# Kernel tuning notes

Measured on AMD Instinct MI355X. Metric: run time of the kernel, lower is better.

## Reference

```python
import jax, jax.numpy as jnp
import numpy as np

E = 8        # n_experts
K = 2        # top_k
D = 1024     # n_embed
H = 2048     # moe_n_hidden
B, T = 4, 2048


def setup_inputs() -> dict:
    key = jax.random.key(0)
    ks = jax.random.split(key, 6)
    s = 0.02
    return {
        "x": jax.random.normal(ks[0], (B, T, D), dtype=jnp.float32),
        "Wr": jax.random.normal(ks[1], (D, E), dtype=jnp.float32) * s,   # router weight
        "W1": jax.random.normal(ks[2], (E, D, 2 * H), dtype=jnp.float32) * s,
        "b1": jnp.zeros((E, 2 * H), dtype=jnp.float32),
        "W2": jax.random.normal(ks[3], (E, H, D), dtype=jnp.float32) * s,
        "b2": jnp.zeros((E, D), dtype=jnp.float32),
    }


def reference(x, Wr, W1, b1, W2, b2):
    b, t, d = x.shape
    # router logits (noise=0, temp=1.0)
    z = jnp.einsum('btd,de->bte', x, Wr)                 # [B,T,E]
    vals, idx = jax.lax.top_k(z, K)                      # [B,T,K]
    gates = jax.nn.softmax(vals, axis=-1)                # [B,T,K]
    # combine weights per (token, expert): sum_k gate_k * 1[idx_k == e]
    onehot = jax.nn.one_hot(idx, E, dtype=x.dtype)       # [B,T,K,E]
    comb = jnp.einsum('btk,btke->bte', gates, onehot).reshape(b * t, E)
    xf = x.reshape(b * t, d)                             # [N,D]
    out = jnp.zeros_like(xf)
    for e in range(E):  # fixed small loop over structurally-distinct experts
        ab = xf @ W1[e] + b1[e]                          # [N,2H]
        a, bb = jnp.split(ab, 2, axis=-1)
        h = jax.nn.silu(a) * bb                          # swiGLU
        y = h @ W2[e] + b2[e]                            # [N,D]
        out = out + comb[:, e:e + 1] * y
    return out.reshape(b, t, d)
```

## Files before the change

### kernel.cpp

```cpp
#include <hip/hip_runtime.h>


#define N_TOK 8192
#define DIM   1024
#define HID   2048
#define NEXP  8
#define NK    (N_TOK * 2)
#define MAXT2 72
#define MAXT1 136

typedef __attribute__((ext_vector_type(8))) short short8;
typedef __attribute__((ext_vector_type(4))) float f32x4;

#define BARX() __builtin_amdgcn_s_barrier()
#define FEN()  asm volatile("" ::: "memory")
#define VMW4() asm volatile("s_waitcnt vmcnt(4)" ::: "memory")
#define VMW2() asm volatile("s_waitcnt vmcnt(2)" ::: "memory")
#define VMW0() asm volatile("s_waitcnt vmcnt(0)" ::: "memory")
#define PRIO(p) __builtin_amdgcn_s_setprio(p)

static __device__ __forceinline__ unsigned short f2bf(float f) {
  unsigned int u = __float_as_uint(f);
  u += 0x7fffu + ((u >> 16) & 1u);
  return (unsigned short)(u >> 16);
}

static __device__ __forceinline__ void glds16(const void* g, void* l) {
  __builtin_amdgcn_global_load_lds(
      (const __attribute__((address_space(1))) unsigned int*)g,
      (__attribute__((address_space(3))) unsigned int*)l, 16, 0, 0);
}

__device__ __forceinline__ void transpose_tile(const float* __restrict__ s,
                                               unsigned short* __restrict__ d,
                                               int R, int C, int c0, int r0,
                                               unsigned short (*tT)[68]) {
  int tid = threadIdx.x;
  int c = tid & 63, rq = tid >> 6;
#pragma unroll
  for (int q = 0; q < 4; ++q) {
    int rb = q * 16 + rq * 4;
    ushort4 v;
    v.x = f2bf(s[(size_t)(r0 + rb + 0) * C + c0 + c]);
    v.y = f2bf(s[(size_t)(r0 + rb + 1) * C + c0 + c]);
    v.z = f2bf(s[(size_t)(r0 + rb + 2) * C + c0 + c]);
    v.w = f2bf(s[(size_t)(r0 + rb + 3) * C + c0 + c]);
    *(ushort4*)&tT[c][rb] = v;
  }
  __syncthreads();
#pragma unroll
  for (int it = 0; it < 4; ++it) {
    int idx = it * 256 + tid;
    int cc = idx >> 4;
    int r4 = (idx & 15) * 4;
    *(ushort4*)(d + (size_t)(c0 + cc) * R + r0 + r4) = *(const ushort4*)&tT[cc][r4];
  }
}

__global__ __launch_bounds__(256) void prep_k(
    const float* __restrict__ x, const float* __restrict__ Wr,
    const float* __restrict__ W1, const float* __restrict__ W2,
    unsigned short* __restrict__ w1t, unsigned short* __restrict__ w2t,
    unsigned short* __restrict__ xb, int* __restrict__ te,
    float* __restrict__ tg, float* __restrict__ out) {
  __shared__ unsigned short tT[64][68];
  int bid = blockIdx.x;
  if (bid < 8192) {
    int z = bid >> 10, rem = bid & 1023;
    int c0 = (rem & 63) * 64, r0 = (rem >> 6) * 64;
    transpose_tile(W1 + (size_t)z * DIM * 2 * HID,
                   w1t + (size_t)z * DIM * 2 * HID, DIM, 2 * HID, c0, r0, tT);
  } else if (bid < 12288) {
    int b2 = bid - 8192;
    int z = b2 >> 9, rem = b2 & 511;
    int c0 = (rem & 15) * 64, r0 = (rem >> 4) * 64;
    transpose_tile(W2 + (size_t)z * HID * DIM,
                   w2t + (size_t)z * HID * DIM, HID, DIM, c0, r0, tT);
  } else if (bid < 14336) {
    int n = (bid - 12288) * 4 + (threadIdx.x >> 6);
    int lane = threadIdx.x & 63;
    float z[8];
#pragma unroll
    for (int e = 0; e < 8; ++e) z[e] = 0.f;
    const float* xr = x + (size_t)n * DIM;
    unsigned short* xbr = xb + (size_t)n * DIM;
#pragma unroll 4
    for (int i = 0; i < DIM / 64; ++i) {
      int d = lane + i * 64;
      float xv = xr[d];
      xbr[d] = f2bf(xv);
      float4 w0 = *(const float4*)(Wr + (size_t)d * 8);
      float4 w1 = *(const float4*)(Wr + (size_t)d * 8 + 4);
      z[0] += xv * w0.x; z[1] += xv * w0.y; z[2] += xv * w0.z; z[3] += xv * w0.w;
      z[4] += xv * w1.x; z[5] += xv * w1.y; z[6] += xv * w1.z; z[7] += xv * w1.w;
    }
    for (int off = 32; off; off >>= 1)
#pragma unroll
      for (int e = 0; e < 8; ++e) z[e] += __shfl_down(z[e], off);
    if (lane == 0) {
      int e0 = 0; float v0 = z[0];
#pragma unroll
      for (int e = 1; e < 8; ++e) if (z[e] > v0) { v0 = z[e]; e0 = e; }
      int e1 = -1; float v1 = -3.4e38f;
#pragma unroll
      for (int e = 0; e < 8; ++e) if (e != e0 && z[e] > v1) { v1 = z[e]; e1 = e; }
      float r = expf(v1 - v0);
      float s0 = 1.f / (1.f + r);
      te[n * 2] = e0; te[n * 2 + 1] = e1;
      tg[n * 2] = s0; tg[n * 2 + 1] = r * s0;
    }
  } else {
    int t = bid - 14336;
    float4* o4 = (float4*)out;
    int idx = t * 256 + threadIdx.x;
#pragma unroll
    for (int i = 0; i < 4; ++i) o4[idx + i * 524288] = (float4){0.f, 0.f, 0.f, 0.f};
  }
}

__global__ __launch_bounds__(1024) void sortscan_k(
    const int* __restrict__ te, const float* __restrict__ tg,
    int* __restrict__ offs, int* __restrict__ tl256, int* __restrict__ tl128,
    int* __restrict__ rows, float* __restrict__ rowg) {
  __shared__ int hist[8];
  __shared__ int curs[8];
  int tid = threadIdx.x;
  if (tid < 8) hist[tid] = 0;
  __syncthreads();
  for (int i = tid; i < NK; i += 1024) atomicAdd(&hist[te[i]], 1);
  __syncthreads();
  if (tid == 0) {
    int o = 0, t2 = 0, t1 = 0;
    offs[0] = 0; tl256[0] = 0; tl128[0] = 0;
    for (int e = 0; e < NEXP; ++e) {
      curs[e] = o;
      o += hist[e];
      offs[e + 1] = o;
      t2 += (hist[e] + 255) >> 8;
      tl256[e + 1] = t2;
      t1 += (hist[e] + 127) >> 7;
      tl128[e + 1] = t1;
    }
  }
  __syncthreads();
  for (int i = tid; i < NK; i += 1024) {
    int e = te[i];
    int pos = atomicAdd(&curs[e], 1);
    rows[pos] = i >> 1;
    rowg[pos] = tg[i];
  }
}

template <int GID, int BM>
__global__ __launch_bounds__(512, 2) void moe_gemm8p(
    const unsigned short* __restrict__ Asrc,
    const unsigned short* __restrict__ Wt,
    const float* __restrict__ bias,
    unsigned short* __restrict__ hb,
    float* __restrict__ out,
    const int* __restrict__ rows,
    const float* __restrict__ rowg,
    const int* __restrict__ offs,
    const int* __restrict__ tl) {
  constexpr int KD = (GID == 0) ? DIM : HID;
  constexpr int NT = KD / 64;
  constexpr int MF = BM / 32;
  constexpr int HBIT = BM / 4;
  constexpr int AG = BM / 128;
  constexpr int ASZ = BM * 64;
  __shared__ unsigned short smem[2 * ASZ + 2 * 16384];

  int bt = blockIdx.x;
  if (bt >= tl[NEXP]) return;
  int e = 0;
  while (e < NEXP - 1 && bt >= tl[e + 1]) ++e;
  int rt = bt - tl[e];
  int base = offs[e];
  int cntE = offs[e + 1] - base;
  int row0 = rt * BM;
  int jb = blockIdx.y;

  int tid = threadIdx.x, lane = tid & 63, w = tid >> 6;
  int wr = w >> 2, wc = w & 3;

  int g8 = (((lane & 7) ^ ((lane >> 3) & 7)) * 8);
  const unsigned short* aP[2][AG];
  const unsigned short* bP[2][2];
  int aD[2][AG], bD[2][2];
#pragma unroll
  for (int hf = 0; hf < 2; ++hf) {
#pragma unroll
    for (int s = 0; s < AG; ++s) {
      int q0 = w * (BM / 16) + s * 8;
      int rbA = (q0 < HBIT ? q0 : q0 + HBIT) + hf * HBIT;
      int rA = rbA + (lane >> 3);
      int rr = row0 + rA; rr = rr < cntE ? rr : cntE - 1;
      if (GID == 0) {
        int tok = rows[base + rr];
        aP[hf][s] = Asrc + (size_t)tok * DIM + g8;
      } else {
        aP[hf][s] = Asrc + (size_t)(base + rr) * HID + g8;
      }
      aD[hf][s] = rbA * 64;
    }
#pragma unroll
    for (int s = 0; s < 2; ++s) {
      int q0 = w * 16 + s * 8;
      int rB = hf * 128 + q0 + (lane >> 3);
      if (GID == 0) {
        int j0h = jb * 128;
        int hcol = j0h + (rB >> 5) * 16 + (rB & 15);
        int w1row = hcol + ((rB >> 4) & 1) * HID;
        bP[hf][s] = Wt + ((size_t)e * 2 * HID + w1row) * DIM + g8;
      } else {
        int j0 = jb * 256;
        bP[hf][s] = Wt + ((size_t)e * DIM + (j0 + rB)) * HID + g8;
      }
      bD[hf][s] = (hf * 128 + q0) * 64;
    }
  }

  auto stA = [&](int t, int hf) {
    if (t < NT) {
#pragma unroll
      for (int s = 0; s < AG; ++s)
        glds16(aP[hf][s] + (size_t)t * 64, smem + (t & 1) * ASZ + aD[hf][s]);
    }
  };
  auto stB = [&](int t, int hf) {
    if (t < NT) {
#pragma unroll
      for (int s = 0; s < 2; ++s)
        glds16(bP[hf][s] + (size_t)t * 64, smem + 2 * ASZ + (t & 1) * 16384 + bD[hf][s]);
    }
  };

  int arow = wr * (BM / 2) + (lane & 15);
  int brow = wc * 64 + (lane & 15);
  int kg = lane >> 4, sx = lane & 7;
  unsigned aoffs[2] = {(unsigned)(arow * 64 + ((kg ^ sx) * 8)),
                       (unsigned)(arow * 64 + (((4 + kg) ^ sx) * 8))};
  unsigned boffs[2] = {(unsigned)(brow * 64 + ((kg ^ sx) * 8)),
                       (unsigned)(brow * 64 + (((4 + kg) ^ sx) * 8))};

  f32x4 acc[MF][4];
#pragma unroll
  for (int m = 0; m < MF; ++m)
#pragma unroll
    for (int n = 0; n < 4; ++n) acc[m][n] = (f32x4){0.f, 0.f, 0.f, 0.f};

  short8 a[2][MF / 2], b[2][4];

#define MFMA_Q(MB, NB)                                                        \
  PRIO(1);                                                                    \
  _Pragma("unroll") for (int ks = 0; ks < 2; ++ks)                            \
  _Pragma("unroll") for (int m = 0; m < MF / 2; ++m)                          \
  _Pragma("unroll") for (int n = 0; n < 2; ++n)                               \
    acc[(MB) + m][(NB) + n] = __builtin_amdgcn_mfma_f32_16x16x32_bf16(        \
        a[ks][m], b[ks][(NB) + n], acc[(MB) + m][(NB) + n], 0, 0, 0);         \
  PRIO(0)

#define GUARD_CNT()                                                           \
  if constexpr (BM == 256) { VMW4(); } else { VMW2(); }

  stA(0, 0); stA(0, 1); stB(0, 0); stB(0, 1); stA(1, 0); stA(1, 1);
  GUARD_CNT(); FEN(); BARX(); FEN();

  for (int it = 0; it < NT / 2; ++it) {
    int T = 2 * it;
    bool notlast = (it < NT / 2 - 1);
#pragma unroll
    for (int half = 0; half < 2; ++half) {
      unsigned Ab = half ? (unsigned)ASZ : 0u;
      unsigned Bb = 2u * ASZ + (half ? 16384u : 0u);
      int Tn = T + half;
#pragma unroll
      for (int ks = 0; ks < 2; ++ks) {
#pragma unroll
        for (int m = 0; m < MF / 2; ++m)
          a[ks][m] = *(const short8*)(smem + Ab + aoffs[ks] + m * 1024);
#pragma unroll
        for (int n = 0; n < 2; ++n)
          b[ks][n] = *(const short8*)(smem + Bb + boffs[ks] + n * 1024);
      }
      stB(Tn + 1, 0);
      FEN(); BARX(); FEN();
      MFMA_Q(0, 0);
      FEN(); BARX(); FEN();
#pragma unroll
      for (int ks = 0; ks < 2; ++ks)
#pragma unroll
        for (int n = 2; n < 4; ++n)
          b[ks][n] = *(const short8*)(smem + Bb + boffs[ks] + n * 1024);
      stB(Tn + 1, 1);
      FEN(); BARX(); FEN();
      MFMA_Q(0, 2);
      FEN(); BARX(); FEN();
#pragma unroll
      for (int ks = 0; ks < 2; ++ks)
#pragma unroll
        for (int m = 0; m < MF / 2; ++m)
          a[ks][m] = *(const short8*)(smem + Ab + aoffs[ks] + (MF / 2 + m) * 1024);
      stA(Tn + 2, 0);
      FEN(); BARX(); FEN();
      MFMA_Q(MF / 2, 2);
      FEN(); BARX(); FEN();
      stA(Tn + 2, 1);
      FEN(); BARX(); FEN();
      MFMA_Q(MF / 2, 0);
      if (half == 0) {
        if (notlast) { GUARD_CNT(); } else { VMW0(); }
      } else {
        GUARD_CNT();
      }
      FEN(); BARX(); FEN();
    }
  }
#undef MFMA_Q
#undef GUARD_CNT

  int rowl = lane >> 4, coll = lane & 15;
  if (GID == 0) {
    int j0h = jb * 128;
#pragma unroll
    for (int pair = 0; pair < 2; ++pair) {
      int hcol = j0h + (2 * wc + pair) * 16 + coll;
      float ba = bias[e * 2 * HID + hcol];
      float bb = bias[e * 2 * HID + HID + hcol];
#pragma unroll
      for (int m = 0; m < MF; ++m)
#pragma unroll
        for (int j = 0; j < 4; ++j) {
          int grow = row0 + wr * (BM / 2) + m * 16 + rowl * 4 + j;
          if (grow < cntE) {
            float av = acc[m][2 * pair][j] + ba;
            float bv = acc[m][2 * pair + 1][j] + bb;
            float hv = av / (1.f + __expf(-av)) * bv;
            hb[(size_t)(base + grow) * HID + hcol] = f2bf(hv);
          }
        }
    }
  } else {
    int j0 = jb * 256;
    float bv[4];
#pragma unroll
    for (int n = 0; n < 4; ++n) bv[n] = bias[e * DIM + j0 + wc * 64 + n * 16 + coll];
#pragma unroll
    for (int m = 0; m < MF; ++m)
#pragma unroll
      for (int j = 0; j < 4; ++j) {
        int grow = row0 + wr * (BM / 2) + m * 16 + rowl * 4 + j;
        if (grow < cntE) {
          int tok = rows[base + grow];
          float g = rowg[base + grow];
#pragma unroll
          for (int n = 0; n < 4; ++n) {
            int col = j0 + wc * 64 + n * 16 + coll;
            atomicAdd(&out[(size_t)tok * DIM + col], g * (acc[m][n][j] + bv[n]));
          }
        }
      }
  }
}

extern "C" void kernel_launch(void* const* d_in, const int* in_sizes, int n_in,
                              void* d_out, int out_size, void* d_ws, size_t ws_size,
                              hipStream_t stream) {
  (void)in_sizes; (void)n_in; (void)out_size;
  const float* x  = (const float*)d_in[0];
  const float* Wr = (const float*)d_in[1];
  const float* W1 = (const float*)d_in[2];
  const float* b1 = (const float*)d_in[3];
  const float* W2 = (const float*)d_in[4];
  const float* b2 = (const float*)d_in[5];
  float* out = (float*)d_out;
  char* ws = (char*)d_ws;

  const size_t o_xb   = 0;
  const size_t o_w1t  = o_xb   + (size_t)N_TOK * DIM * 2;
  const size_t o_w2t  = o_w1t  + (size_t)NEXP * 2 * HID * DIM * 2;
  const size_t o_hb   = o_w2t  + (size_t)NEXP * DIM * HID * 2;
  const size_t o_rows = o_hb   + (size_t)NK * HID * 2;
  const size_t o_rowg = o_rows + (size_t)NK * 4;
  const size_t o_te   = o_rowg + (size_t)NK * 4;
  const size_t o_tg   = o_te   + (size_t)NK * 4;
  const size_t o_offs = o_tg   + (size_t)NK * 4;
  const size_t o_t2   = o_offs + 64;
  const size_t o_t1   = o_t2   + 64;
  const size_t need   = o_t1   + 64;
  if (ws_size < need) return;

  unsigned short* xb  = (unsigned short*)(ws + o_xb);
  unsigned short* w1t = (unsigned short*)(ws + o_w1t);
  unsigned short* w2t = (unsigned short*)(ws + o_w2t);
  unsigned short* hb  = (unsigned short*)(ws + o_hb);
  int*   rows = (int*)(ws + o_rows);
  float* rowg = (float*)(ws + o_rowg);
  int*   te   = (int*)(ws + o_te);
  float* tg   = (float*)(ws + o_tg);
  int*   offs = (int*)(ws + o_offs);
  int*   tl256 = (int*)(ws + o_t2);
  int*   tl128 = (int*)(ws + o_t1);

  prep_k<<<16384, 256, 0, stream>>>(x, Wr, W1, W2, w1t, w2t, xb, te, tg, out);
  sortscan_k<<<1, 1024, 0, stream>>>(te, tg, offs, tl256, tl128, rows, rowg);
  moe_gemm8p<0, 256><<<dim3(MAXT2, HID / 128), 512, 0, stream>>>(
      xb, w1t, b1, hb, nullptr, rows, rowg, offs, tl256);
  moe_gemm8p<1, 128><<<dim3(MAXT1, DIM / 256), 512, 0, stream>>>(
      hb, w2t, b2, nullptr, out, rows, rowg, offs, tl128);
}
```

Measured before the change: 419.3 us.

## Switch grouped MoE GEMMs from 16x16x32 to 32x32x16 bf16 MFMA tiles

Both expert GEMM kernels now use the 32x32x16 bf16 MFMA instruction instead of 16x16x32. The per-wave fragment layout, LDS read offsets, W1 gate/up row interleave, and epilogue row/column mapping are rewritten for the 32-wide output tiles. Larger MFMA tiles cut LDS fragment reads per FLOP and the instruction count. The trade-offs are more register pressure from 16-float accumulators and an extra lgkmcnt wait inside the pipeline.

```diff
diff --git a/kernel.cpp b/kernel.cpp
--- a/kernel.cpp
+++ b/kernel.cpp
@@ -10,13 +10,14 @@
 #define MAXT1 136
 
 typedef __attribute__((ext_vector_type(8))) short short8;
-typedef __attribute__((ext_vector_type(4))) float f32x4;
+typedef __attribute__((ext_vector_type(16))) float f32x16;
 
 #define BARX() __builtin_amdgcn_s_barrier()
 #define FEN()  asm volatile("" ::: "memory")
 #define VMW4() asm volatile("s_waitcnt vmcnt(4)" ::: "memory")
 #define VMW2() asm volatile("s_waitcnt vmcnt(2)" ::: "memory")
 #define VMW0() asm volatile("s_waitcnt vmcnt(0)" ::: "memory")
+#define LGKM0() asm volatile("s_waitcnt lgkmcnt(0)" ::: "memory")
 #define PRIO(p) __builtin_amdgcn_s_setprio(p)
 
 static __device__ __forceinline__ unsigned short f2bf(float f) {
@@ -152,7 +153,7 @@
 }
 
 template <int GID, int BM>
-__global__ __launch_bounds__(512, 2) void moe_gemm8p(
+__global__ __launch_bounds__(512, 2) void moe_gemm32(
     const unsigned short* __restrict__ Asrc,
     const unsigned short* __restrict__ Wt,
     const float* __restrict__ bias,
@@ -164,9 +165,8 @@
     const int* __restrict__ tl) {
   constexpr int KD = (GID == 0) ? DIM : HID;
   constexpr int NT = KD / 64;
-  constexpr int MF = BM / 32;
-  constexpr int HBIT = BM / 4;
-  constexpr int AG = BM / 128;
+  constexpr int MW = BM / 64;
+  constexpr int MH = MW / 2;
   constexpr int ASZ = BM * 64;
   __shared__ unsigned short smem[2 * ASZ + 2 * 16384];
 
@@ -184,16 +184,43 @@
   int wr = w >> 2, wc = w & 3;
 
   int g8 = (((lane & 7) ^ ((lane >> 3) & 7)) * 8);
+  const unsigned short* bP[2][2];
+  int bD[2][2];
+#pragma unroll
+  for (int hf = 0; hf < 2; ++hf)
+#pragma unroll
+    for (int s = 0; s < 2; ++s) {
+      int q0 = w * 16 + s * 8;
+      int rB = hf * 128 + q0 + (lane >> 3);
+      if (GID == 0) {
+        int g = rB >> 6, rr = rB & 63;
+        int hcol = jb * 128 + g * 32 + (rr & 31);
+        int w1row = hcol + (rr >> 5) * HID;
+        bP[hf][s] = Wt + ((size_t)e * 2 * HID + w1row) * DIM + g8;
+      } else {
+        int j0 = jb * 256;
+        bP[hf][s] = Wt + ((size_t)e * DIM + (j0 + rB)) * HID + g8;
+      }
+      bD[hf][s] = (hf * 128 + q0) * 64;
+    }
+  constexpr int AG = (BM == 256) ? 2 : 1;
+  constexpr int HBIT = BM / 4;
   const unsigned short* aP[2][AG];
-  const unsigned short* bP[2][2];
-  int aD[2][AG], bD[2][2];
-#pragma unroll
-  for (int hf = 0; hf < 2; ++hf) {
+  int aD[2][AG];
+#pragma unroll
+  for (int hf = 0; hf < 2; ++hf)
 #pragma unroll
     for (int s = 0; s < AG; ++s) {
-      int q0 = w * (BM / 16) + s * 8;
-      int rbA = (q0 < HBIT ? q0 : q0 + HBIT) + hf * HBIT;
-      int rA = rbA + (lane >> 3);
+      int rbA, rA;
+      if (BM == 256) {
+        int q0 = w * 16 + s * 8;
+        rbA = (q0 < HBIT ? q0 : q0 + HBIT) + hf * HBIT;
+        rA = rbA + (lane >> 3);
+      } else {
+        int q0 = w * 8;
+        rbA = (q0 < HBIT ? q0 : q0 + HBIT) + hf * HBIT;
+        rA = rbA + (lane >> 3);
+      }
       int rr = row0 + rA; rr = rr < cntE ? rr : cntE - 1;
       if (GID == 0) {
         int tok = rows[base + rr];
@@ -203,22 +230,6 @@
       }
       aD[hf][s] = rbA * 64;
     }
-#pragma unroll
-    for (int s = 0; s < 2; ++s) {
-      int q0 = w * 16 + s * 8;
-      int rB = hf * 128 + q0 + (lane >> 3);
-      if (GID == 0) {
-        int j0h = jb * 128;
-        int hcol = j0h + (rB >> 5) * 16 + (rB & 15);
-        int w1row = hcol + ((rB >> 4) & 1) * HID;
-        bP[hf][s] = Wt + ((size_t)e * 2 * HID + w1row) * DIM + g8;
-      } else {
-        int j0 = jb * 256;
-        bP[hf][s] = Wt + ((size_t)e * DIM + (j0 + rB)) * HID + g8;
-      }
-      bD[hf][s] = (hf * 128 + q0) * 64;
-    }
-  }
 
   auto stA = [&](int t, int hf) {
     if (t < NT) {
@@ -235,129 +246,149 @@
     }
   };
 
-  int arow = wr * (BM / 2) + (lane & 15);
-  int brow = wc * 64 + (lane & 15);
-  int kg = lane >> 4, sx = lane & 7;
-  unsigned aoffs[2] = {(unsigned)(arow * 64 + ((kg ^ sx) * 8)),
-                       (unsigned)(arow * 64 + (((4 + kg) ^ sx) * 8))};
-  unsigned boffs[2] = {(unsigned)(brow * 64 + ((kg ^ sx) * 8)),
-                       (unsigned)(brow * 64 + (((4 + kg) ^ sx) * 8))};
-
-  f32x4 acc[MF][4];
-#pragma unroll
-  for (int m = 0; m < MF; ++m)
-#pragma unroll
-    for (int n = 0; n < 4; ++n) acc[m][n] = (f32x4){0.f, 0.f, 0.f, 0.f};
-
-  short8 a[2][MF / 2], b[2][4];
-
-#define MFMA_Q(MB, NB)                                                        \
-  PRIO(1);                                                                    \
-  _Pragma("unroll") for (int ks = 0; ks < 2; ++ks)                            \
-  _Pragma("unroll") for (int m = 0; m < MF / 2; ++m)                          \
-  _Pragma("unroll") for (int n = 0; n < 2; ++n)                               \
-    acc[(MB) + m][(NB) + n] = __builtin_amdgcn_mfma_f32_16x16x32_bf16(        \
-        a[ks][m], b[ks][(NB) + n], acc[(MB) + m][(NB) + n], 0, 0, 0);         \
-  PRIO(0)
-
-#define GUARD_CNT()                                                           \
-  if constexpr (BM == 256) { VMW4(); } else { VMW2(); }
+  unsigned aBase = (unsigned)((wr * (BM / 2) + (lane & 31)) * 64);
+  unsigned bBase = (unsigned)((wc * 64 + (lane & 31)) * 64);
+  int kx[4];
+#pragma unroll
+  for (int ks = 0; ks < 4; ++ks)
+    kx[ks] = ((2 * ks + (lane >> 5)) ^ (lane & 7)) * 8;
+
+  f32x16 acc[MW][2];
+#pragma unroll
+  for (int m = 0; m < MW; ++m)
+#pragma unroll
+    for (int n = 0; n < 2; ++n)
+#pragma unroll
+      for (int j = 0; j < 16; ++j) acc[m][n][j] = 0.f;
+
+  short8 aL0[MH][2], aL1[MH][2], aHH[MH][4], bL[2][2], bHi[2][2];
+
+#define GUARD() if constexpr (GID == 0) { VMW4(); } else { VMW2(); }
 
   stA(0, 0); stA(0, 1); stB(0, 0); stB(0, 1); stA(1, 0); stA(1, 1);
-  GUARD_CNT(); FEN(); BARX(); FEN();
+  GUARD(); FEN(); BARX(); FEN();
 
   for (int it = 0; it < NT / 2; ++it) {
-    int T = 2 * it;
-    bool notlast = (it < NT / 2 - 1);
 #pragma unroll
     for (int half = 0; half < 2; ++half) {
+      int Tn = 2 * it + half;
       unsigned Ab = half ? (unsigned)ASZ : 0u;
       unsigned Bb = 2u * ASZ + (half ? 16384u : 0u);
-      int Tn = T + half;
-#pragma unroll
-      for (int ks = 0; ks < 2; ++ks) {
-#pragma unroll
-        for (int m = 0; m < MF / 2; ++m)
-          a[ks][m] = *(const short8*)(smem + Ab + aoffs[ks] + m * 1024);
-#pragma unroll
-        for (int n = 0; n < 2; ++n)
-          b[ks][n] = *(const short8*)(smem + Bb + boffs[ks] + n * 1024);
+#pragma unroll
+      for (int m = 0; m < MH; ++m)
+#pragma unroll
+        for (int ks = 0; ks < 2; ++ks)
+          aL0[m][ks] = *(const short8*)(smem + Ab + aBase + m * 2048 + kx[ks]);
+#pragma unroll
+      for (int n = 0; n < 2; ++n)
+#pragma unroll
+        for (int ks = 0; ks < 2; ++ks)
+          bL[n][ks] = *(const short8*)(smem + Bb + bBase + n * 2048 + kx[ks]);
+      stB(Tn + 1, 0);
+      FEN(); BARX(); FEN();
+      PRIO(1);
+#pragma unroll
+      for (int ks = 0; ks < 2; ++ks)
+#pragma unroll
+        for (int m = 0; m < MH; ++m)
+#pragma unroll
+          for (int n = 0; n < 2; ++n)
+            acc[m][n] = __builtin_amdgcn_mfma_f32_32x32x16_bf16(
+                aL0[m][ks], bL[n][ks], acc[m][n], 0, 0, 0);
+      PRIO(0);
+      FEN(); BARX(); FEN();
+#pragma unroll
+      for (int m = 0; m < MH; ++m)
+#pragma unroll
+        for (int ks = 0; ks < 2; ++ks)
+          aL1[m][ks] = *(const short8*)(smem + Ab + aBase + m * 2048 + kx[2 + ks]);
+#pragma unroll
+      for (int n = 0; n < 2; ++n)
+#pragma unroll
+        for (int ks = 0; ks < 2; ++ks)
+          bHi[n][ks] = *(const short8*)(smem + Bb + bBase + n * 2048 + kx[2 + ks]);
+      stB(Tn + 1, 1);
+      FEN(); BARX(); FEN();
+      PRIO(1);
+#pragma unroll
+      for (int ks = 0; ks < 2; ++ks)
+#pragma unroll
+        for (int m = 0; m < MH; ++m)
+#pragma unroll
+          for (int n = 0; n < 2; ++n)
+            acc[m][n] = __builtin_amdgcn_mfma_f32_32x32x16_bf16(
+                aL1[m][ks], bHi[n][ks], acc[m][n], 0, 0, 0);
+      PRIO(0);
+      FEN(); BARX(); FEN();
+#pragma unroll
+      for (int m = 0; m < MH; ++m)
+#pragma unroll
+        for (int ks = 0; ks < 4; ++ks)
+          aHH[m][ks] = *(const short8*)(smem + Ab + aBase + (MH + m) * 2048 + kx[ks]);
+      stA(Tn + 2, 0);
+      FEN(); BARX(); FEN();
+      PRIO(1);
+#pragma unroll
+      for (int ks = 0; ks < 2; ++ks)
+#pragma unroll
+        for (int m = 0; m < MH; ++m)
+#pragma unroll
+          for (int n = 0; n < 2; ++n)
+            acc[MH + m][n] = __builtin_amdgcn_mfma_f32_32x32x16_bf16(
+                aHH[m][ks], bL[n][ks], acc[MH + m][n], 0, 0, 0);
+      PRIO(0);
+      LGKM0();
+      FEN(); BARX(); FEN();
+      stA(Tn + 2, 1);
+      FEN(); BARX(); FEN();
+      PRIO(1);
+#pragma unroll
+      for (int ks = 0; ks < 2; ++ks)
+#pragma unroll
+        for (int m = 0; m < MH; ++m)
+#pragma unroll
+          for (int n = 0; n < 2; ++n)
+            acc[MH + m][n] = __builtin_amdgcn_mfma_f32_32x32x16_bf16(
+                aHH[m][2 + ks], bHi[n][ks], acc[MH + m][n], 0, 0, 0);
+      PRIO(0);
+      if (Tn + 2 < NT) { GUARD(); } else { VMW0(); }
+      FEN(); BARX(); FEN();
+    }
+  }
+#undef GUARD
+
+  int cc = lane & 31;
+  int rhi = (lane >> 5) * 4;
+  if (GID == 0) {
+    int hcol = jb * 128 + wc * 32 + cc;
+    float ba = bias[e * 2 * HID + hcol];
+    float bbv = bias[e * 2 * HID + HID + hcol];
+#pragma unroll
+    for (int m = 0; m < MW; ++m)
+#pragma unroll
+      for (int reg = 0; reg < 16; ++reg) {
+        int grow = row0 + wr * (BM / 2) + m * 32 + (reg & 3) + 8 * (reg >> 2) + rhi;
+        if (grow < cntE) {
+          float av = acc[m][0][reg] + ba;
+          float bv = acc[m][1][reg] + bbv;
+          float hv = av / (1.f + __expf(-av)) * bv;
+          hb[(size_t)(base + grow) * HID + hcol] = f2bf(hv);
+        }
       }
-      stB(Tn + 1, 0);
-      FEN(); BARX(); FEN();
-      MFMA_Q(0, 0);
-      FEN(); BARX(); FEN();
-#pragma unroll
-      for (int ks = 0; ks < 2; ++ks)
-#pragma unroll
-        for (int n = 2; n < 4; ++n)
-          b[ks][n] = *(const short8*)(smem + Bb + boffs[ks] + n * 1024);
-      stB(Tn + 1, 1);
-      FEN(); BARX(); FEN();
-      MFMA_Q(0, 2);
-      FEN(); BARX(); FEN();
-#pragma unroll
-      for (int ks = 0; ks < 2; ++ks)
-#pragma unroll
-        for (int m = 0; m < MF / 2; ++m)
-          a[ks][m] = *(const short8*)(smem + Ab + aoffs[ks] + (MF / 2 + m) * 1024);
-      stA(Tn + 2, 0);
-      FEN(); BARX(); FEN();
-      MFMA_Q(MF / 2, 2);
-      FEN(); BARX(); FEN();
-      stA(Tn + 2, 1);
-      FEN(); BARX(); FEN();
-      MFMA_Q(MF / 2, 0);
-      if (half == 0) {
-        if (notlast) { GUARD_CNT(); } else { VMW0(); }
-      } else {
-        GUARD_CNT();
-      }
-      FEN(); BARX(); FEN();
-    }
-  }
-#undef MFMA_Q
-#undef GUARD_CNT
-
-  int rowl = lane >> 4, coll = lane & 15;
-  if (GID == 0) {
-    int j0h = jb * 128;
-#pragma unroll
-    for (int pair = 0; pair < 2; ++pair) {
-      int hcol = j0h + (2 * wc + pair) * 16 + coll;
-      float ba = bias[e * 2 * HID + hcol];
-      float bb = bias[e * 2 * HID + HID + hcol];
-#pragma unroll
-      for (int m = 0; m < MF; ++m)
-#pragma unroll
-        for (int j = 0; j < 4; ++j) {
-          int grow = row0 + wr * (BM / 2) + m * 16 + rowl * 4 + j;
-          if (grow < cntE) {
-            float av = acc[m][2 * pair][j] + ba;
-            float bv = acc[m][2 * pair + 1][j] + bb;
-            float hv = av / (1.f + __expf(-av)) * bv;
-            hb[(size_t)(base + grow) * HID + hcol] = f2bf(hv);
-          }
-        }
-    }
   } else {
-    int j0 = jb * 256;
-    float bv[4];
-#pragma unroll
-    for (int n = 0; n < 4; ++n) bv[n] = bias[e * DIM + j0 + wc * 64 + n * 16 + coll];
-#pragma unroll
-    for (int m = 0; m < MF; ++m)
-#pragma unroll
-      for (int j = 0; j < 4; ++j) {
-        int grow = row0 + wr * (BM / 2) + m * 16 + rowl * 4 + j;
+    int col0 = jb * 256 + wc * 64;
+    float bv0 = bias[e * DIM + col0 + cc];
+    float bv1 = bias[e * DIM + col0 + 32 + cc];
+#pragma unroll
+    for (int m = 0; m < MW; ++m)
+#pragma unroll
+      for (int reg = 0; reg < 16; ++reg) {
+        int grow = row0 + wr * (BM / 2) + m * 32 + (reg & 3) + 8 * (reg >> 2) + rhi;
         if (grow < cntE) {
           int tok = rows[base + grow];
           float g = rowg[base + grow];
-#pragma unroll
-          for (int n = 0; n < 4; ++n) {
-            int col = j0 + wc * 64 + n * 16 + coll;
-            atomicAdd(&out[(size_t)tok * DIM + col], g * (acc[m][n][j] + bv[n]));
-          }
+          atomicAdd(&out[(size_t)tok * DIM + col0 + cc], g * (acc[m][0][reg] + bv0));
+          atomicAdd(&out[(size_t)tok * DIM + col0 + 32 + cc], g * (acc[m][1][reg] + bv1));
         }
       }
   }
@@ -404,8 +435,8 @@
 
   prep_k<<<16384, 256, 0, stream>>>(x, Wr, W1, W2, w1t, w2t, xb, te, tg, out);
   sortscan_k<<<1, 1024, 0, stream>>>(te, tg, offs, tl256, tl128, rows, rowg);
-  moe_gemm8p<0, 256><<<dim3(MAXT2, HID / 128), 512, 0, stream>>>(
+  moe_gemm32<0, 256><<<dim3(MAXT2, HID / 128), 512, 0, stream>>>(
       xb, w1t, b1, hb, nullptr, rows, rowg, offs, tl256);
-  moe_gemm8p<1, 128><<<dim3(MAXT1, DIM / 256), 512, 0, stream>>>(
+  moe_gemm32<1, 128><<<dim3(MAXT1, DIM / 256), 512, 0, stream>>>(
       hb, w2t, b2, nullptr, out, rows, rowg, offs, tl128);
 }
```

Result: slower. 440.5 us (+5.1%).
